# Kernel optimization log

Hardware: AMD Instinct MI355X
Metric: run time of the kernel (lower is better)

Reference implementation:

```python
import jax, jax.numpy as jnp
import numpy as np

B, L, D, K = 4, 512, 768, 96
H = 4 * D  # projection hidden width


def _proj(x, w1, b1, w2, b2):
    # create_projection_layer: Linear -> ReLU -> (Dropout, identity at eval) -> Linear
    return jnp.maximum(x @ w1 + b1, 0.0) @ w2 + b2


def setup_inputs() -> dict:
    key = jax.random.key(0)
    ks = jax.random.split(key, 12)
    g = lambda k, shape, fan: jax.random.normal(k, shape, jnp.float32) * (1.0 / np.sqrt(fan))
    inp = {
        "h": jax.random.normal(ks[0], (B, L, D), jnp.float32),
        "span_idx": jax.random.randint(ks[1], (B, K, 2), 0, L),
        "ps_w1": g(ks[2], (D, H), D), "ps_b1": jnp.zeros((H,), jnp.float32),
        "ps_w2": g(ks[3], (H, D), H), "ps_b2": jnp.zeros((D,), jnp.float32),
        "pe_w1": g(ks[4], (D, H), D), "pe_b1": jnp.zeros((H,), jnp.float32),
        "pe_w2": g(ks[5], (H, D), H), "pe_b2": jnp.zeros((D,), jnp.float32),
        "so_w1": g(ks[6], (2 * D, H), 2 * D), "so_b1": jnp.zeros((H,), jnp.float32),
        "so_w2": g(ks[7], (H, D), H), "so_b2": jnp.zeros((D,), jnp.float32),
        "ro_w1": g(ks[8], (2 * D, H), 2 * D), "ro_b1": jnp.zeros((H,), jnp.float32),
        "ro_w2": g(ks[9], (H, D), H), "ro_b2": jnp.zeros((D,), jnp.float32),
    }
    return inp


def _gather_tokens(rep, idx):
    # rep: [B,L,D], idx: [B,K] -> [B,K,D]
    b, k = idx.shape
    d = rep.shape[-1]
    return jnp.take_along_axis(rep, jnp.broadcast_to(idx[:, :, None], (b, k, d)), axis=1)


def reference(h, span_idx, ps_w1, ps_b1, ps_w2, ps_b2, pe_w1, pe_b1, pe_w2, pe_b2,
              so_w1, so_b1, so_w2, so_b2, ro_w1, ro_b1, ro_w2, ro_b2):
    # SpanMarkerV1
    start_rep = _proj(h, ps_w1, ps_b1, ps_w2, ps_b2)   # [B,L,D]
    end_rep = _proj(h, pe_w1, pe_b1, pe_w2, pe_b2)     # [B,L,D]
    st = _gather_tokens(start_rep, span_idx[:, :, 0])  # [B,K,D]
    en = _gather_tokens(end_rep, span_idx[:, :, 1])    # [B,K,D]
    cat = jnp.maximum(jnp.concatenate([st, en], axis=-1), 0.0)  # relu
    entity_reps = _proj(cat, so_w1, so_b1, so_w2, so_b2)        # [B,K,D]

    # off-diagonal pair enumeration, row-major (i,j) with i != j — static indices
    n = entity_reps.shape[1]
    idx = np.arange(n)
    ii = np.repeat(idx, n)
    jj = np.tile(idx, n)
    keep = ii != jj
    ii, jj = ii[keep], jj[keep]  # each length n*(n-1)
    pairs = jnp.concatenate([entity_reps[:, ii], entity_reps[:, jj]], axis=-1)  # [B,P,2D]
    return _proj(pairs, ro_w1, ro_b1, ro_w2, ro_b2)  # [B,P,D]
```

## Files before the change

### kernel.cpp

```cpp
#include <hip/hip_runtime.h>
#include <hip/hip_bf16.h>

#define Bdim 4
#define Ldim 512
#define Ddim 768
#define Kspan 96
#define Hdim 3072
#define Pdim 9120
#define MROWS 384
#define NT6 96

typedef __bf16 bf16x8 __attribute__((ext_vector_type(8)));
typedef float f32x4 __attribute__((ext_vector_type(4)));
typedef float f32x16 __attribute__((ext_vector_type(16)));
typedef unsigned short ushort8v __attribute__((ext_vector_type(8)));

static __device__ __forceinline__ unsigned short f2bf(float x){
  return __builtin_bit_cast(unsigned short, (__bf16)x);
}
static __device__ __forceinline__ float bf2f(unsigned short u){
  return (float)__builtin_bit_cast(__bf16, u);
}
static __device__ __forceinline__ float bfbits2f(unsigned short u){
  return __builtin_bit_cast(float, (unsigned)u << 16);
}

struct TJob { const float* W; unsigned short* Th; unsigned short* Tl; int K; int N; int base; };
struct TJobs { TJob j[7]; };

__global__ __launch_bounds__(256) void transpose_multi(TJobs JJ)
{
  int x = blockIdx.x;
  int ji = 0;
  #pragma unroll
  for (int q = 1; q < 7; q++) if (x >= JJ.j[q].base) ji = q;
  TJob J = JJ.j[ji];
  int local = x - J.base;
  int tilesX = J.N >> 6;
  int bx = local % tilesX, by = local / tilesX;
  __shared__ float tile[64][65];
  int k0 = by * 64, n0 = bx * 64;
  int c = threadIdx.x & 63, r0 = threadIdx.x >> 6;
  for (int p = 0; p < 16; p++){
    int r = r0 + p * 4;
    tile[c][r] = J.W[(size_t)(k0 + r) * J.N + n0 + c];
  }
  __syncthreads();
  for (int p = 0; p < 16; p++){
    int n = r0 + p * 4;
    float xv = tile[n][c];
    unsigned short h = f2bf(xv);
    size_t o = (size_t)(n0 + n) * J.K + k0 + c;
    J.Th[o] = h;
    J.Tl[o] = f2bf(xv - bf2f(h));
  }
}

__global__ __launch_bounds__(256) void pack_w2(
    const float* __restrict__ W, unsigned short* __restrict__ W2P)
{
  __shared__ float tile[32][129];
  int kt = blockIdx.x, nq = blockIdx.y, t = threadIdx.x;
  for (int q = 0; q < 16; q++){
    int flat = q * 256 + t;
    int kl = flat >> 7, n = flat & 127;
    tile[kl][n] = W[(size_t)(kt * 32 + kl) * Ddim + nq * 128 + n];
  }
  __syncthreads();
  unsigned short* outp = W2P + (size_t)(nq * 96 + kt) * 4096;
  for (int q = 0; q < 16; q++){
    int o = q * 256 + t;
    int n = o >> 5, slot = (o >> 3) & 3, e = o & 7;
    int kl = (slot ^ ((n >> 1) & 3)) * 8 + e;
    outp[o] = f2bf(tile[kl][n]);
  }
}

__global__ __launch_bounds__(256) void gather_rows(
    const float* __restrict__ h, const int* __restrict__ span, float* __restrict__ hg)
{
  int x = blockIdx.x;
  int sel = (x >= MROWS) ? 1 : 0;
  int r = x - sel * MROWS;
  int b = r / Kspan, k = r - b * Kspan;
  int idx = span[(b * Kspan + k) * 2 + sel];
  const float* src = h + ((size_t)b * Ldim + idx) * Ddim;
  float* dst = hg + (size_t)x * Ddim;
  for (int d = threadIdx.x; d < Ddim; d += 256) dst[d] = src[d];
}

struct GJob {
  const float* A;
  const unsigned short* Wh;
  const unsigned short* Wl;
  const float* bias;
  float* C;
};

template<int MODE, int SPLIT>
__global__ __launch_bounds__(256) void gemm_ms(
    GJob j0, GJob j1, int ldA, int ldW, int ldC, int kLen, size_t csz)
{
  constexpr int SR = 40;
  __shared__ __align__(16) unsigned short Ah[64 * SR], Al[64 * SR];
  __shared__ __align__(16) unsigned short Bh[128 * SR], Bl[128 * SR];
  int zj, s;
  if (SPLIT == 1){ zj = blockIdx.z; s = 0; }
  else { zj = blockIdx.z / SPLIT; s = blockIdx.z % SPLIT; }
  const GJob J = zj ? j1 : j0;
  int kBegin = s * kLen;
  float* Cptr = (MODE == 2) ? (J.C + (size_t)s * csz) : J.C;

  int m0 = blockIdx.y * 64, n0 = blockIdx.x * 128;
  int t = threadIdx.x, lane = t & 63, wid = t >> 6;
  int wm = wid >> 1, wn = wid & 1;
  int lr = lane & 15, lk = (lane >> 4) * 8;
  f32x4 acc[2][4] = {};
  int ar = t >> 2, akq = t & 3;
  for (int k0 = 0; k0 < kLen; k0 += 32){
    {
      const float* sp = J.A + (size_t)(m0 + ar) * ldA + kBegin + k0 + akq * 8;
      f32x4 x0 = *(const f32x4*)sp, x1 = *(const f32x4*)(sp + 4);
      ushort8v vh, vl;
      for (int e = 0; e < 4; e++){ float x = x0[e]; unsigned short hh = f2bf(x); vh[e] = hh; vl[e] = f2bf(x - bf2f(hh)); }
      for (int e = 0; e < 4; e++){ float x = x1[e]; unsigned short hh = f2bf(x); vh[e+4] = hh; vl[e+4] = f2bf(x - bf2f(hh)); }
      *(ushort8v*)&Ah[ar * SR + akq * 8] = vh;
      *(ushort8v*)&Al[ar * SR + akq * 8] = vl;
    }
    for (int p = 0; p < 2; p++){
      int idx = p * 256 + t; int n = idx >> 2, kq = idx & 3;
      size_t go = (size_t)(n0 + n) * ldW + kBegin + k0 + kq * 8;
      *(ushort8v*)&Bh[n * SR + kq * 8] = *(const ushort8v*)(J.Wh + go);
      *(ushort8v*)&Bl[n * SR + kq * 8] = *(const ushort8v*)(J.Wl + go);
    }
    __syncthreads();
    bf16x8 ah[2], al2[2], bh[4], bl[4];
    for (int f = 0; f < 2; f++){ int o = (wm * 32 + f * 16 + lr) * SR + lk; ah[f] = *(const bf16x8*)&Ah[o]; al2[f] = *(const bf16x8*)&Al[o]; }
    for (int g = 0; g < 4; g++){ int o = (wn * 64 + g * 16 + lr) * SR + lk; bh[g] = *(const bf16x8*)&Bh[o]; bl[g] = *(const bf16x8*)&Bl[o]; }
    for (int f = 0; f < 2; f++)
      for (int g = 0; g < 4; g++){
        acc[f][g] = __builtin_amdgcn_mfma_f32_16x16x32_bf16(ah[f],  bh[g], acc[f][g], 0, 0, 0);
        acc[f][g] = __builtin_amdgcn_mfma_f32_16x16x32_bf16(ah[f],  bl[g], acc[f][g], 0, 0, 0);
        acc[f][g] = __builtin_amdgcn_mfma_f32_16x16x32_bf16(al2[f], bh[g], acc[f][g], 0, 0, 0);
      }
    __syncthreads();
  }
  int rr = (lane >> 4) * 4;
  for (int f = 0; f < 2; f++){
    int gm = m0 + wm * 32 + f * 16 + rr;
    for (int g = 0; g < 4; g++){
      int gn = n0 + wn * 64 + g * 16 + (lane & 15);
      float bv = ((MODE == 0 || MODE == 1) && J.bias) ? J.bias[gn] : 0.f;
      if (MODE == 5 && zj == 0) bv = J.bias[gn];
      for (int r2 = 0; r2 < 4; r2++){
        float v = acc[f][g][r2] + bv;
        if (MODE == 0) v = fmaxf(v, 0.f);
        if (MODE == 5 && zj == 1){
          ((unsigned short*)J.C)[(size_t)(gm + r2) * ldC + gn] = f2bf(v);
        } else {
          Cptr[(size_t)(gm + r2) * ldC + gn] = v;
        }
      }
    }
  }
}

template<bool RELU>
__global__ __launch_bounds__(256) void reduce_part(
    const float* __restrict__ P, int S,
    const float* __restrict__ bias0, const float* __restrict__ bias1,
    float* __restrict__ outp, int zCount, int ldOut)
{
  const int MN = MROWS * Ddim;
  int idx4 = blockIdx.x * 256 + threadIdx.x;
  int flat = idx4 * 4;
  if (flat >= MN * zCount) return;
  int z = flat / MN; int rem = flat - z * MN;
  int r = rem / Ddim; int c = rem - r * Ddim;
  const float* base = P + (size_t)z * S * MN + rem;
  f32x4 sv = *(const f32x4*)base;
  for (int ss = 1; ss < S; ss++){ f32x4 v = *(const f32x4*)(base + (size_t)ss * MN); sv += v; }
  const float* bp = z ? bias1 : bias0;
  f32x4 bv = *(const f32x4*)(bp + c);
  sv += bv;
  if (RELU) for (int e = 0; e < 4; e++) sv[e] = fmaxf(sv[e], 0.f);
  *(f32x4*)(outp + (size_t)r * ldOut + z * Ddim + c) = sv;
}

__global__ __launch_bounds__(256, 2) void pair_gemm7(
    const float* __restrict__ U,
    const unsigned short* __restrict__ Vp,
    const unsigned short* __restrict__ W2P,
    const float* __restrict__ b2,
    float* __restrict__ out)
{
  __shared__ __align__(16) unsigned short As[2][192 * 32];
  __shared__ __align__(16) unsigned short Bs[2][128 * 32];
  __shared__ __align__(16) float Uls[2][Hdim];

  int x = blockIdx.x;
  int xcd = x & 7;
  int s = x >> 3;
  int grp = s / 48;
  int ig  = s - grp * 48;
  int combo = xcd + grp * 8;
  int nq = combo % 6, b = combo / 6;

  int t = threadIdx.x, lane = t & 63, w = t >> 6;
  int wm = w >> 1, wn = w & 1;
  int l31 = lane & 31, hsel = lane >> 5;
  int i0 = ig * 2, i = i0 + wm;

  int brow = t >> 2, bg = t & 3;
  int vj[3];
  #pragma unroll
  for (int q = 0; q < 3; q++){
    int r = brow + 64 * q;
    vj[q] = (r >= 96) ? (r - 96) : r;
  }

  f32x16 acc[3][2] = {};
  ushort8v vE[3], vO[3];

  auto loadV = [&](int kt, ushort8v* dst){
    #pragma unroll
    for (int q = 0; q < 3; q++)
      dst[q] = *(const ushort8v*)(Vp + (size_t)(b * 96 + vj[q]) * Hdim + kt * 32 + bg * 8);
  };
  auto issueB = [&](int kt, int buf){
    const unsigned short* src = W2P + (size_t)(nq * 96 + kt) * 4096 + t * 8;
    unsigned short* d0 = (buf == 0) ? &Bs[0][t * 8] : &Bs[1][t * 8];
    __builtin_amdgcn_global_load_lds(
        (const __attribute__((address_space(1))) unsigned int*)src,
        (__attribute__((address_space(3))) unsigned int*)d0, 16, 0, 0);
    __builtin_amdgcn_global_load_lds(
        (const __attribute__((address_space(1))) unsigned int*)(src + 2048),
        (__attribute__((address_space(3))) unsigned int*)(d0 + 2048), 16, 0, 0);
  };
  auto build = [&](int kt, int buf, ushort8v* vsrc){
    #pragma unroll
    for (int q = 0; q < 3; q++){
      int r = brow + 64 * q;
      int ihalf = (r >= 96) ? 1 : 0;
      const float* up = &Uls[ihalf][kt * 32 + bg * 8];
      f32x4 ua = *(const f32x4*)up;
      f32x4 ub = *(const f32x4*)(up + 4);
      ushort8v vv = vsrc[q];
      ushort8v pk;
      #pragma unroll
      for (int e = 0; e < 4; e++) pk[e]     = f2bf(fmaxf(ua[e] + bfbits2f(vv[e]),     0.f));
      #pragma unroll
      for (int e = 0; e < 4; e++) pk[e + 4] = f2bf(fmaxf(ub[e] + bfbits2f(vv[e + 4]), 0.f));
      unsigned short* dp = (buf == 0) ? &As[0][0] : &As[1][0];
      *(ushort8v*)(dp + r * 32 + ((bg ^ ((r >> 1) & 3)) << 3)) = pk;
    }
  };
  auto compute = [&](int buf){
    const unsigned short* ap = (buf == 0) ? &As[0][0] : &As[1][0];
    const unsigned short* bp = (buf == 0) ? &Bs[0][0] : &Bs[1][0];
    #pragma unroll
    for (int kh = 0; kh < 2; kh++){
      int g = kh * 2 + hsel;
      bf16x8 bfr[2], afr[3];
      #pragma unroll
      for (int nf = 0; nf < 2; nf++){
        int n = wn * 64 + nf * 32 + l31;
        bfr[nf] = *(const bf16x8*)(bp + n * 32 + ((g ^ ((n >> 1) & 3)) << 3));
      }
      #pragma unroll
      for (int mf = 0; mf < 3; mf++){
        int r = wm * 96 + mf * 32 + l31;
        afr[mf] = *(const bf16x8*)(ap + r * 32 + ((g ^ ((r >> 1) & 3)) << 3));
      }
      #pragma unroll
      for (int mf = 0; mf < 3; mf++)
        #pragma unroll
        for (int nf = 0; nf < 2; nf++)
          acc[mf][nf] = __builtin_amdgcn_mfma_f32_32x32x16_bf16(afr[mf], bfr[nf], acc[mf][nf], 0, 0, 0);
    }
  };

  loadV(0, vE);
  issueB(0, 0);
  {
    const float* u0 = U + (size_t)(b * 96 + i0) * Hdim;
    for (int q = t; q < 2 * (Hdim / 4); q += 256){
      int r = q / (Hdim / 4), c = q - r * (Hdim / 4);
      *(f32x4*)&Uls[r][c * 4] = *(const f32x4*)(u0 + (size_t)r * Hdim + c * 4);
    }
  }
  __syncthreads();
  build(0, 0, vE);
  loadV(1, vO);
  __syncthreads();

  for (int kt = 0; kt < NT6; kt += 2){
    if (kt + 1 < NT6) issueB(kt + 1, 1);
    if (kt + 2 < NT6) loadV(kt + 2, vE);
    if (kt + 1 < NT6) build(kt + 1, 1, vO);
    compute(0);
    __syncthreads();
    int ko = kt + 1;
    if (ko + 1 < NT6) issueB(ko + 1, 0);
    if (ko + 2 < NT6) loadV(ko + 2, vO);
    if (ko + 1 < NT6) build(ko + 1, 0, vE);
    compute(1);
    __syncthreads();
  }

  size_t outB = (size_t)b * Pdim;
  int colbase = nq * 128 + wn * 64;
  float bc[2];
  #pragma unroll
  for (int nf = 0; nf < 2; nf++) bc[nf] = b2[colbase + nf * 32 + l31];
  #pragma unroll
  for (int mf = 0; mf < 3; mf++){
    #pragma unroll
    for (int reg = 0; reg < 16; reg++){
      int j = mf * 32 + (reg & 3) + 8 * (reg >> 2) + 4 * hsel;
      if (j == i) continue;
      int p = i * 95 + j - (j > i ? 1 : 0);
      float* orow = out + (outB + p) * Ddim + colbase;
      #pragma unroll
      for (int nf = 0; nf < 2; nf++)
        orow[nf * 32 + l31] = acc[mf][nf][reg] + bc[nf];
    }
  }
}

extern "C" void kernel_launch(void* const* d_in, const int* in_sizes, int n_in,
                              void* d_out, int out_size, void* d_ws, size_t ws_size,
                              hipStream_t stream)
{
  (void)in_sizes; (void)n_in; (void)out_size;
  const float* h     = (const float*)d_in[0];
  const int*   span  = (const int*)d_in[1];
  const float* ps_w1 = (const float*)d_in[2];
  const float* ps_b1 = (const float*)d_in[3];
  const float* ps_w2 = (const float*)d_in[4];
  const float* ps_b2 = (const float*)d_in[5];
  const float* pe_w1 = (const float*)d_in[6];
  const float* pe_b1 = (const float*)d_in[7];
  const float* pe_w2 = (const float*)d_in[8];
  const float* pe_b2 = (const float*)d_in[9];
  const float* so_w1 = (const float*)d_in[10];
  const float* so_b1 = (const float*)d_in[11];
  const float* so_w2 = (const float*)d_in[12];
  const float* so_b2 = (const float*)d_in[13];
  const float* ro_w1 = (const float*)d_in[14];
  const float* ro_b1 = (const float*)d_in[15];
  const float* ro_w2 = (const float*)d_in[16];
  const float* ro_b2 = (const float*)d_in[17];

  char* ws = (char*)d_ws;
  size_t off = 0;
  auto alloc_us = [&](size_t n)->unsigned short*{
    unsigned short* p = (unsigned short*)(ws + off);
    off += ((n * 2 + 255) & ~(size_t)255);
    return p;
  };
  auto alloc_f = [&](size_t n)->float*{
    float* p = (float*)(ws + off);
    off += ((n * 4 + 255) & ~(size_t)255);
    return p;
  };

  unsigned short* ps1h = alloc_us((size_t)Hdim * Ddim); unsigned short* ps1l = alloc_us((size_t)Hdim * Ddim);
  unsigned short* ps2h = alloc_us((size_t)Ddim * Hdim); unsigned short* ps2l = alloc_us((size_t)Ddim * Hdim);
  unsigned short* pe1h = alloc_us((size_t)Hdim * Ddim); unsigned short* pe1l = alloc_us((size_t)Hdim * Ddim);
  unsigned short* pe2h = alloc_us((size_t)Ddim * Hdim); unsigned short* pe2l = alloc_us((size_t)Ddim * Hdim);
  unsigned short* so1h = alloc_us((size_t)Hdim * 2 * Ddim); unsigned short* so1l = alloc_us((size_t)Hdim * 2 * Ddim);
  unsigned short* so2h = alloc_us((size_t)Ddim * Hdim); unsigned short* so2l = alloc_us((size_t)Ddim * Hdim);
  unsigned short* ro1h = alloc_us((size_t)Hdim * 2 * Ddim); unsigned short* ro1l = alloc_us((size_t)Hdim * 2 * Ddim);
  unsigned short* W2P  = alloc_us((size_t)6 * 96 * 4096);
  unsigned short* Vp   = alloc_us((size_t)MROWS * Hdim);
  float* hg     = alloc_f((size_t)2 * MROWS * Ddim);
  float* mid_s  = alloc_f((size_t)MROWS * Hdim);
  float* mid_e  = alloc_f((size_t)MROWS * Hdim);
  float* cat    = alloc_f((size_t)MROWS * 2 * Ddim);
  float* entity = alloc_f((size_t)MROWS * Ddim);
  float* Ubuf   = alloc_f((size_t)MROWS * Hdim);
  const size_t MN = (size_t)MROWS * Ddim;
  float* P2 = alloc_f(8 * MN);
  float* P3 = alloc_f(8 * MN);
  if (off > ws_size) return;

  dim3 tb(256);

  {
    TJobs JJ;
    int base = 0;
    auto add = [&](int idx, const float* W, unsigned short* Th, unsigned short* Tl, int K, int N){
      JJ.j[idx] = TJob{W, Th, Tl, K, N, base};
      base += (N / 64) * (K / 64);
    };
    add(0, ps_w1, ps1h, ps1l, Ddim, Hdim);
    add(1, ps_w2, ps2h, ps2l, Hdim, Ddim);
    add(2, pe_w1, pe1h, pe1l, Ddim, Hdim);
    add(3, pe_w2, pe2h, pe2l, Hdim, Ddim);
    add(4, so_w1, so1h, so1l, 2 * Ddim, Hdim);
    add(5, so_w2, so2h, so2l, Hdim, Ddim);
    add(6, ro_w1, ro1h, ro1l, 2 * Ddim, Hdim);
    transpose_multi<<<base, tb, 0, stream>>>(JJ);
  }
  pack_w2<<<dim3(NT6, 6), tb, 0, stream>>>(ro_w2, W2P);

  gather_rows<<<2 * MROWS, tb, 0, stream>>>(h, span, hg);

  {
    GJob j0{hg,                      ps1h, ps1l, ps_b1, mid_s};
    GJob j1{hg + (size_t)MROWS*Ddim, pe1h, pe1l, pe_b1, mid_e};
    gemm_ms<0,1><<<dim3(Hdim/128, MROWS/64, 2), tb, 0, stream>>>(j0, j1, Ddim, Ddim, Hdim, Ddim, 0);
  }
  {
    GJob j0{mid_s, ps2h, ps2l, nullptr, P2};
    GJob j1{mid_e, pe2h, pe2l, nullptr, P2 + 4*MN};
    gemm_ms<2,4><<<dim3(Ddim/128, MROWS/64, 8), tb, 0, stream>>>(j0, j1, Hdim, Hdim, Ddim, Hdim/4, MN);
  }
  reduce_part<true><<<(2*(int)MN)/1024, tb, 0, stream>>>(P2, 4, ps_b2, pe_b2, cat, 2, 2*Ddim);
  {
    GJob j0{cat, so1h, so1l, so_b1, mid_s};
    gemm_ms<0,1><<<dim3(Hdim/128, MROWS/64, 1), tb, 0, stream>>>(j0, j0, 2*Ddim, 2*Ddim, Hdim, 2*Ddim, 0);
  }
  {
    GJob j0{mid_s, so2h, so2l, nullptr, P3};
    gemm_ms<2,8><<<dim3(Ddim/128, MROWS/64, 8), tb, 0, stream>>>(j0, j0, Hdim, Hdim, Ddim, Hdim/8, MN);
  }
  reduce_part<false><<<((int)MN)/1024, tb, 0, stream>>>(P3, 8, so_b2, so_b2, entity, 1, Ddim);
  {
    GJob j0{entity, ro1h,        ro1l,        ro_b1,  Ubuf};
    GJob j1{entity, ro1h + Ddim, ro1l + Ddim, nullptr, (float*)Vp};
    gemm_ms<5,1><<<dim3(Hdim/128, MROWS/64, 2), tb, 0, stream>>>(j0, j1, Ddim, 2*Ddim, Hdim, Ddim, 0);
  }

  pair_gemm7<<<1152, tb, 0, stream>>>(Ubuf, Vp, W2P, ro_b2, (float*)d_out);
}
```

Baseline: 490.6 us.

## Load W2 fragments directly to registers and store U as bf16

```diff
diff --git a/kernel.cpp b/kernel.cpp
--- a/kernel.cpp
+++ b/kernel.cpp
@@ -57,7 +57,7 @@
 }
 
 __global__ __launch_bounds__(256) void pack_w2(
-    const float* __restrict__ W, unsigned short* __restrict__ W2P)
+    const float* __restrict__ W, unsigned short* __restrict__ W2B)
 {
   __shared__ float tile[32][129];
   int kt = blockIdx.x, nq = blockIdx.y, t = threadIdx.x;
@@ -67,12 +67,14 @@
     tile[kl][n] = W[(size_t)(kt * 32 + kl) * Ddim + nq * 128 + n];
   }
   __syncthreads();
-  unsigned short* outp = W2P + (size_t)(nq * 96 + kt) * 4096;
+  unsigned short* outp = W2B + (size_t)(nq * 96 + kt) * 4096;
   for (int q = 0; q < 16; q++){
     int o = q * 256 + t;
-    int n = o >> 5, slot = (o >> 3) & 3, e = o & 7;
-    int kl = (slot ^ ((n >> 1) & 3)) * 8 + e;
-    outp[o] = f2bf(tile[kl][n]);
+    int wn = (o >> 11) & 1, kh = (o >> 10) & 1, nf = (o >> 9) & 1;
+    int hs = (o >> 8) & 1, l31 = (o >> 3) & 31, e = o & 7;
+    int nl = wn * 64 + nf * 32 + l31;
+    int kl = (kh * 2 + hs) * 8 + e;
+    outp[o] = f2bf(tile[kl][nl]);
   }
 }
 
@@ -150,12 +152,11 @@
     int gm = m0 + wm * 32 + f * 16 + rr;
     for (int g = 0; g < 4; g++){
       int gn = n0 + wn * 64 + g * 16 + (lane & 15);
-      float bv = ((MODE == 0 || MODE == 1) && J.bias) ? J.bias[gn] : 0.f;
-      if (MODE == 5 && zj == 0) bv = J.bias[gn];
+      float bv = (MODE != 2 && J.bias) ? J.bias[gn] : 0.f;
       for (int r2 = 0; r2 < 4; r2++){
         float v = acc[f][g][r2] + bv;
         if (MODE == 0) v = fmaxf(v, 0.f);
-        if (MODE == 5 && zj == 1){
+        if (MODE == 6){
           ((unsigned short*)J.C)[(size_t)(gm + r2) * ldC + gn] = f2bf(v);
         } else {
           Cptr[(size_t)(gm + r2) * ldC + gn] = v;
@@ -187,16 +188,14 @@
   *(f32x4*)(outp + (size_t)r * ldOut + z * Ddim + c) = sv;
 }
 
-__global__ __launch_bounds__(256, 2) void pair_gemm7(
-    const float* __restrict__ U,
+__global__ __launch_bounds__(256, 2) void pair_gemm8(
+    const unsigned short* __restrict__ Ub,
     const unsigned short* __restrict__ Vp,
-    const unsigned short* __restrict__ W2P,
+    const unsigned short* __restrict__ W2B,
     const float* __restrict__ b2,
     float* __restrict__ out)
 {
   __shared__ __align__(16) unsigned short As[2][192 * 32];
-  __shared__ __align__(16) unsigned short Bs[2][128 * 32];
-  __shared__ __align__(16) float Uls[2][Hdim];
 
   int x = blockIdx.x;
   int xcd = x & 7;
@@ -212,61 +211,59 @@
   int i0 = ig * 2, i = i0 + wm;
 
   int brow = t >> 2, bg = t & 3;
-  int vj[3];
+  int vj[3], ih[3];
   #pragma unroll
   for (int q = 0; q < 3; q++){
     int r = brow + 64 * q;
     vj[q] = (r >= 96) ? (r - 96) : r;
+    ih[q] = (r >= 96) ? 1 : 0;
   }
 
   f32x16 acc[3][2] = {};
-  ushort8v vE[3], vO[3];
-
-  auto loadV = [&](int kt, ushort8v* dst){
+  ushort8v vE[3], vO[3], uE[2], uO[2], bE[4], bO[4];
+
+  const unsigned short* Vbase = Vp + (size_t)(b * 96) * Hdim + bg * 8;
+  const unsigned short* Ubase = Ub + (size_t)(b * 96 + i0) * Hdim + bg * 8;
+  const unsigned short* Wt = W2B + (size_t)(nq * 96) * 4096 + wn * 2048 + hsel * 256 + l31 * 8;
+
+  auto loadVU = [&](int kt, ushort8v* v, ushort8v* u){
     #pragma unroll
     for (int q = 0; q < 3; q++)
-      dst[q] = *(const ushort8v*)(Vp + (size_t)(b * 96 + vj[q]) * Hdim + kt * 32 + bg * 8);
-  };
-  auto issueB = [&](int kt, int buf){
-    const unsigned short* src = W2P + (size_t)(nq * 96 + kt) * 4096 + t * 8;
-    unsigned short* d0 = (buf == 0) ? &Bs[0][t * 8] : &Bs[1][t * 8];
-    __builtin_amdgcn_global_load_lds(
-        (const __attribute__((address_space(1))) unsigned int*)src,
-        (__attribute__((address_space(3))) unsigned int*)d0, 16, 0, 0);
-    __builtin_amdgcn_global_load_lds(
-        (const __attribute__((address_space(1))) unsigned int*)(src + 2048),
-        (__attribute__((address_space(3))) unsigned int*)(d0 + 2048), 16, 0, 0);
-  };
-  auto build = [&](int kt, int buf, ushort8v* vsrc){
+      v[q] = *(const ushort8v*)(Vbase + (size_t)vj[q] * Hdim + kt * 32);
+    u[0] = *(const ushort8v*)(Ubase + kt * 32);
+    u[1] = *(const ushort8v*)(Ubase + Hdim + kt * 32);
+  };
+  auto loadB = [&](int kt, ushort8v* dst){
+    const unsigned short* p = Wt + (size_t)kt * 4096;
+    dst[0] = *(const ushort8v*)(p);
+    dst[1] = *(const ushort8v*)(p + 512);
+    dst[2] = *(const ushort8v*)(p + 1024);
+    dst[3] = *(const ushort8v*)(p + 1536);
+  };
+  auto build = [&](int buf, const ushort8v* v, const ushort8v* u){
+    float uf[2][8];
+    #pragma unroll
+    for (int h2 = 0; h2 < 2; h2++)
+      #pragma unroll
+      for (int e = 0; e < 8; e++) uf[h2][e] = bfbits2f(u[h2][e]);
+    unsigned short* dp = (buf == 0) ? &As[0][0] : &As[1][0];
     #pragma unroll
     for (int q = 0; q < 3; q++){
       int r = brow + 64 * q;
-      int ihalf = (r >= 96) ? 1 : 0;
-      const float* up = &Uls[ihalf][kt * 32 + bg * 8];
-      f32x4 ua = *(const f32x4*)up;
-      f32x4 ub = *(const f32x4*)(up + 4);
-      ushort8v vv = vsrc[q];
+      ushort8v vv = v[q];
       ushort8v pk;
       #pragma unroll
-      for (int e = 0; e < 4; e++) pk[e]     = f2bf(fmaxf(ua[e] + bfbits2f(vv[e]),     0.f));
-      #pragma unroll
-      for (int e = 0; e < 4; e++) pk[e + 4] = f2bf(fmaxf(ub[e] + bfbits2f(vv[e + 4]), 0.f));
-      unsigned short* dp = (buf == 0) ? &As[0][0] : &As[1][0];
+      for (int e = 0; e < 8; e++)
+        pk[e] = f2bf(fmaxf(uf[ih[q]][e] + bfbits2f(vv[e]), 0.f));
       *(ushort8v*)(dp + r * 32 + ((bg ^ ((r >> 1) & 3)) << 3)) = pk;
     }
   };
-  auto compute = [&](int buf){
+  auto compute = [&](int buf, const ushort8v* bfrag){
     const unsigned short* ap = (buf == 0) ? &As[0][0] : &As[1][0];
-    const unsigned short* bp = (buf == 0) ? &Bs[0][0] : &Bs[1][0];
     #pragma unroll
     for (int kh = 0; kh < 2; kh++){
       int g = kh * 2 + hsel;
-      bf16x8 bfr[2], afr[3];
-      #pragma unroll
-      for (int nf = 0; nf < 2; nf++){
-        int n = wn * 64 + nf * 32 + l31;
-        bfr[nf] = *(const bf16x8*)(bp + n * 32 + ((g ^ ((n >> 1) & 3)) << 3));
-      }
+      bf16x8 afr[3];
       #pragma unroll
       for (int mf = 0; mf < 3; mf++){
         int r = wm * 96 + mf * 32 + l31;
@@ -276,35 +273,34 @@
       for (int mf = 0; mf < 3; mf++)
         #pragma unroll
         for (int nf = 0; nf < 2; nf++)
-          acc[mf][nf] = __builtin_amdgcn_mfma_f32_32x32x16_bf16(afr[mf], bfr[nf], acc[mf][nf], 0, 0, 0);
-    }
-  };
-
-  loadV(0, vE);
-  issueB(0, 0);
-  {
-    const float* u0 = U + (size_t)(b * 96 + i0) * Hdim;
-    for (int q = t; q < 2 * (Hdim / 4); q += 256){
-      int r = q / (Hdim / 4), c = q - r * (Hdim / 4);
-      *(f32x4*)&Uls[r][c * 4] = *(const f32x4*)(u0 + (size_t)r * Hdim + c * 4);
-    }
-  }
+          acc[mf][nf] = __builtin_amdgcn_mfma_f32_32x32x16_bf16(
+              afr[mf], __builtin_bit_cast(bf16x8, bfrag[kh * 2 + nf]), acc[mf][nf], 0, 0, 0);
+    }
+  };
+
+  loadVU(0, vE, uE); loadB(0, bE);
+  loadVU(1, vO, uO); loadB(1, bO);
+  build(0, vE, uE);
   __syncthreads();
-  build(0, 0, vE);
-  loadV(1, vO);
-  __syncthreads();
 
   for (int kt = 0; kt < NT6; kt += 2){
-    if (kt + 1 < NT6) issueB(kt + 1, 1);
-    if (kt + 2 < NT6) loadV(kt + 2, vE);
-    if (kt + 1 < NT6) build(kt + 1, 1, vO);
-    compute(0);
+    ushort8v tb[4];
+    if (kt + 2 < NT6){ loadVU(kt + 2, vE, uE); loadB(kt + 2, tb); }
+    if (kt + 1 < NT6) build(1, vO, uO);
+    compute(0, bE);
+    if (kt + 2 < NT6){
+      #pragma unroll
+      for (int q = 0; q < 4; q++) bE[q] = tb[q];
+    }
     __syncthreads();
     int ko = kt + 1;
-    if (ko + 1 < NT6) issueB(ko + 1, 0);
-    if (ko + 2 < NT6) loadV(ko + 2, vO);
-    if (ko + 1 < NT6) build(ko + 1, 0, vE);
-    compute(1);
+    if (ko + 2 < NT6){ loadVU(ko + 2, vO, uO); loadB(ko + 2, tb); }
+    if (ko + 1 < NT6) build(0, vE, uE);
+    compute(1, bO);
+    if (ko + 2 < NT6){
+      #pragma unroll
+      for (int q = 0; q < 4; q++) bO[q] = tb[q];
+    }
     __syncthreads();
   }
 
@@ -372,14 +368,14 @@
   unsigned short* so1h = alloc_us((size_t)Hdim * 2 * Ddim); unsigned short* so1l = alloc_us((size_t)Hdim * 2 * Ddim);
   unsigned short* so2h = alloc_us((size_t)Ddim * Hdim); unsigned short* so2l = alloc_us((size_t)Ddim * Hdim);
   unsigned short* ro1h = alloc_us((size_t)Hdim * 2 * Ddim); unsigned short* ro1l = alloc_us((size_t)Hdim * 2 * Ddim);
-  unsigned short* W2P  = alloc_us((size_t)6 * 96 * 4096);
+  unsigned short* W2B  = alloc_us((size_t)6 * 96 * 4096);
   unsigned short* Vp   = alloc_us((size_t)MROWS * Hdim);
+  unsigned short* Ub   = alloc_us((size_t)MROWS * Hdim);
   float* hg     = alloc_f((size_t)2 * MROWS * Ddim);
   float* mid_s  = alloc_f((size_t)MROWS * Hdim);
   float* mid_e  = alloc_f((size_t)MROWS * Hdim);
   float* cat    = alloc_f((size_t)MROWS * 2 * Ddim);
   float* entity = alloc_f((size_t)MROWS * Ddim);
-  float* Ubuf   = alloc_f((size_t)MROWS * Hdim);
   const size_t MN = (size_t)MROWS * Ddim;
   float* P2 = alloc_f(8 * MN);
   float* P3 = alloc_f(8 * MN);
@@ -403,7 +399,7 @@
     add(6, ro_w1, ro1h, ro1l, 2 * Ddim, Hdim);
     transpose_multi<<<base, tb, 0, stream>>>(JJ);
   }
-  pack_w2<<<dim3(NT6, 6), tb, 0, stream>>>(ro_w2, W2P);
+  pack_w2<<<dim3(NT6, 6), tb, 0, stream>>>(ro_w2, W2B);
 
   gather_rows<<<2 * MROWS, tb, 0, stream>>>(h, span, hg);
 
@@ -428,10 +424,10 @@
   }
   reduce_part<false><<<((int)MN)/1024, tb, 0, stream>>>(P3, 8, so_b2, so_b2, entity, 1, Ddim);
   {
-    GJob j0{entity, ro1h,        ro1l,        ro_b1,  Ubuf};
+    GJob j0{entity, ro1h,        ro1l,        ro_b1,  (float*)Ub};
     GJob j1{entity, ro1h + Ddim, ro1l + Ddim, nullptr, (float*)Vp};
-    gemm_ms<5,1><<<dim3(Hdim/128, MROWS/64, 2), tb, 0, stream>>>(j0, j1, Ddim, 2*Ddim, Hdim, Ddim, 0);
-  }
-
-  pair_gemm7<<<1152, tb, 0, stream>>>(Ubuf, Vp, W2P, ro_b2, (float*)d_out);
-}
+    gemm_ms<6,1><<<dim3(Hdim/128, MROWS/64, 2), tb, 0, stream>>>(j0, j1, Ddim, 2*Ddim, Hdim, Ddim, 0);
+  }
+
+  pair_gemm8<<<1152, tb, 0, stream>>>(Ub, Vp, W2B, ro_b2, (float*)d_out);
+}
```

Measured after the change: 1.045 ms. 113% more time.
